# Kernel tuning notes

Measured on AMD Instinct MI355X. Metric: run time of the kernel, lower is better.

## Reference

```python
import jax, jax.numpy as jnp
import numpy as np

B, T, E, H, D = 1, 2048, 1024, 16, 64  # H*D == E required by module


def setup_inputs() -> dict:
    key = jax.random.key(0)
    ks = jax.random.split(key, 9)
    s_in = (2.0 / E) ** 0.5
    return {
        "x": jax.random.normal(ks[0], (B, T, E), jnp.float32),
        "wq": jax.random.normal(ks[1], (H * D, E), jnp.float32) * E ** -0.5,
        "wk": jax.random.normal(ks[2], (H * D, E), jnp.float32) * E ** -0.5,
        "wv": jax.random.normal(ks[3], (H * D, E), jnp.float32) * E ** -0.5,
        "wr": jax.random.normal(ks[4], (H, E, T), jnp.float32) * s_in,
        "wvr": jax.random.normal(ks[5], (H * D, E), jnp.float32) * E ** -0.5,
        "wj": jax.random.normal(ks[6], (E, E), jnp.float32) * E ** -0.5,
        "gate": jnp.zeros((H, 3), jnp.float32),
        "wo": jax.random.normal(ks[7], (E, H * D), jnp.float32) * E ** -0.5,
    }


def reference(x, wq, wk, wv, wr, wvr, wj, gate, wo):
    Bx, Tx, Ex = x.shape
    Hh = wr.shape[0]
    Dd = wq.shape[0] // Hh
    scale = 1.0 / Dd ** 0.5
    neg = -jnp.inf
    mask = jnp.triu(jnp.ones((Tx, Tx), bool), 1)  # True above diagonal

    def heads(w):  # (B,T,H*D) -> (B,H,T,D)
        return (x @ w.T).reshape(Bx, Tx, Hh, Dd).transpose(0, 2, 1, 3)

    # --- branch 1: standard causal QKV attention ---
    q, k, v = heads(wq), heads(wk), heads(wv)
    qkv_attn = jnp.einsum('bhqd,bhkd->bhqk', q, k) * scale
    qkv_attn = jnp.where(mask, neg, qkv_attn)
    qkv_out = jnp.einsum('bhqk,bhkd->bhqd', jax.nn.softmax(qkv_attn, axis=-1), v)

    # --- branch 2: RRPRAM learned per-position scores ---
    rv = heads(wvr)
    r = jnp.einsum('bte,het->bht', x, wr[:, :, :Tx])  # (B,H,T) key scores
    r_attn = jnp.where(mask, neg, (r * scale)[:, :, None, :])  # (B,H,T,T)
    rrp_out = jnp.einsum('bhqk,bhkd->bhqd', jax.nn.softmax(r_attn, axis=-1), rv)

    # --- branch 3: Janus self-resonance ---
    echo = x @ wj.T            # (B,T,E)
    echo_back = echo @ wj      # F.linear(echo, wj.weight.T)
    scores = (x * echo_back).sum(-1) / Ex ** 0.5  # (B,T)
    j_attn = jnp.where(mask, neg, scores[:, :, None] * scores[:, None, :])  # (B,T,T)
    jA = jax.nn.softmax(j_attn, axis=-1)
    j_val = echo.reshape(Bx, Tx, Hh, Dd).transpose(0, 2, 1, 3)
    jan_out = jnp.einsum('bqk,bhkd->bhqd', jA, j_val)

    # --- gated combine + output proj ---
    g = jax.nn.softmax(gate, axis=-1)  # (H,3)
    out = (g[:, 0][None, :, None, None] * qkv_out
           + g[:, 1][None, :, None, None] * rrp_out
           + g[:, 2][None, :, None, None] * jan_out)
    out = out.transpose(0, 2, 1, 3).reshape(Bx, Tx, Hh * Dd)
    return out @ wo.T
```

## Files before the change

kernel.cpp:

```cpp
#include <hip/hip_runtime.h>
#include <cstddef>
#include <cstdint>

#define TT 2048
#define EE 1024
#define HH 16

typedef unsigned short ushort;
typedef unsigned int uint;
typedef __attribute__((ext_vector_type(8))) short short8;
typedef __attribute__((ext_vector_type(8))) _Float16 half8;
typedef __attribute__((ext_vector_type(4))) float f32x4;
typedef __attribute__((ext_vector_type(4))) ushort ushort4v;

__device__ __forceinline__ ushort f2bf(float f) {
  uint u = __builtin_bit_cast(uint, f);
  u = (u + 0x7FFFu + ((u >> 16) & 1u)) >> 16;
  return (ushort)u;
}
__device__ __forceinline__ float bf2f(ushort h) {
  return __builtin_bit_cast(float, (uint)h << 16);
}

__device__ __forceinline__ void async16(ushort* lds, const ushort* g) {
  __builtin_amdgcn_global_load_lds(
      reinterpret_cast<const __attribute__((address_space(1))) void*>(
          reinterpret_cast<uintptr_t>(g)),
      reinterpret_cast<__attribute__((address_space(3))) void*>(
          static_cast<unsigned int>(reinterpret_cast<uintptr_t>(lds))),
      16, 0, 0);
}

__global__ __launch_bounds__(256) void cvt_x_k(
    const float* __restrict__ in, ushort* __restrict__ obf,
    ushort* __restrict__ oh, float* __restrict__ snorm, int n) {
  if (blockIdx.x == 0) {
    for (int i = threadIdx.x; i < TT; i += 256) snorm[i] = 0.f;
  }
  int i = (blockIdx.x * 256 + threadIdx.x) * 4;
  if (i >= n) return;
  float4 v = *(const float4*)(in + i);
  ushort4v b, h;
  b.x = f2bf(v.x); b.y = f2bf(v.y); b.z = f2bf(v.z); b.w = f2bf(v.w);
  h.x = __builtin_bit_cast(ushort, (_Float16)v.x);
  h.y = __builtin_bit_cast(ushort, (_Float16)v.y);
  h.z = __builtin_bit_cast(ushort, (_Float16)v.z);
  h.w = __builtin_bit_cast(ushort, (_Float16)v.w);
  *(ushort4v*)(obf + i) = b;
  *(ushort4v*)(oh + i) = h;
}

__global__ __launch_bounds__(256) void cvt_w_k(
    const float* __restrict__ s0, const float* __restrict__ s1,
    const float* __restrict__ s2, const float* __restrict__ s3,
    const float* __restrict__ s4, const float* __restrict__ s5,
    ushort* __restrict__ d0, ushort* __restrict__ d1,
    ushort* __restrict__ d2, ushort* __restrict__ d3,
    ushort* __restrict__ d4, ushort* __restrict__ d5, int n) {
  const int which = blockIdx.y;
  const float* src; ushort* dst;
  switch (which) {
    case 0: src = s0; dst = d0; break;
    case 1: src = s1; dst = d1; break;
    case 2: src = s2; dst = d2; break;
    case 3: src = s3; dst = d3; break;
    case 4: src = s4; dst = d4; break;
    default: src = s5; dst = d5; break;
  }
  int i = (blockIdx.x * 256 + threadIdx.x) * 4;
  if (i >= n) return;
  float4 v = *(const float4*)(src + i);
  ushort4v o;
  if (which == 5) {
    o.x = __builtin_bit_cast(ushort, (_Float16)v.x);
    o.y = __builtin_bit_cast(ushort, (_Float16)v.y);
    o.z = __builtin_bit_cast(ushort, (_Float16)v.z);
    o.w = __builtin_bit_cast(ushort, (_Float16)v.w);
  } else {
    o.x = f2bf(v.x); o.y = f2bf(v.y); o.z = f2bf(v.z); o.w = f2bf(v.w);
  }
  *(ushort4v*)(dst + i) = o;
}

__global__ __launch_bounds__(256) void transpose_k(
    const float* __restrict__ in, float* __restrict__ outT, int M, int N)
{
  __shared__ float tile[32][33];
  const int bn = blockIdx.x * 32;
  const int bm = blockIdx.y * 32;
  const int tx = threadIdx.x & 31, ty = threadIdx.x >> 5;
#pragma unroll
  for (int i = 0; i < 32; i += 8)
    tile[ty + i][tx] = in[(size_t)(bm + ty + i) * N + bn + tx];
  __syncthreads();
#pragma unroll
  for (int i = 0; i < 32; i += 8)
    outT[(size_t)(bn + ty + i) * M + bm + tx] = tile[tx][ty + i];
}

__global__ __launch_bounds__(256) void proj5(
    const ushort* __restrict__ Abf, const ushort* __restrict__ Ah,
    const ushort* __restrict__ B0, const ushort* __restrict__ B1,
    const ushort* __restrict__ B2, const ushort* __restrict__ B3,
    const ushort* __restrict__ B4,
    ushort* __restrict__ C0, ushort* __restrict__ C1,
    ushort* __restrict__ C2, ushort* __restrict__ C3,
    ushort* __restrict__ C4, float* __restrict__ snorm,
    int M, int N, int K)
{
  const ushort* A; const ushort* B; ushort* C; int om;
  switch (blockIdx.z) {
    case 0: A = Abf; B = B0; C = C0; om = 1; break;
    case 1: A = Abf; B = B1; C = C1; om = 1; break;
    case 2: A = Abf; B = B2; C = C2; om = 2; break;
    case 3: A = Abf; B = B3; C = C3; om = 1; break;
    default: A = Ah; B = B4; C = C4; om = 3; break;
  }
  const bool f16 = (blockIdx.z == 4);
  __shared__ __align__(16) ushort As[2][128 * 64];
  __shared__ __align__(16) ushort Bs[2][128 * 64];
  const int tid = threadIdx.x;
  const int m0 = blockIdx.y * 128, n0 = blockIdx.x * 128;
  const int w = tid >> 6, lane = tid & 63;
  const int wr = w >> 1, wc = w & 1;
  const int lr = lane & 15, lk = lane >> 4;
  const int srow = lane >> 3;
  const int scol = ((lane & 7) ^ srow) * 8;
  const ushort* AgL = A + (size_t)(m0 + w * 32 + srow) * K + scol;
  const ushort* BgL = B + (size_t)(n0 + w * 32 + srow) * K + scol;
  const int sbase = (w * 32) * 64;
  const int s0 = (lk ^ (lr & 7)) * 8;
  f32x4 acc[4][4] = {};
  const int NT = K >> 6;
#pragma unroll
  for (int c = 0; c < 4; ++c) {
    async16(&As[0][sbase + c * 8 * 64], AgL + (size_t)c * 8 * K);
    async16(&Bs[0][sbase + c * 8 * 64], BgL + (size_t)c * 8 * K);
  }
  __syncthreads();
  for (int kt = 0; kt < NT; ++kt) {
    const int cur = kt & 1;
    if (kt + 1 < NT) {
      const int kn = (kt + 1) << 6;
#pragma unroll
      for (int c = 0; c < 4; ++c) {
        async16(&As[cur ^ 1][sbase + c * 8 * 64], AgL + (size_t)c * 8 * K + kn);
        async16(&Bs[cur ^ 1][sbase + c * 8 * 64], BgL + (size_t)c * 8 * K + kn);
      }
    }
    short8 a0[4], a1[4], b0[4], b1[4];
#pragma unroll
    for (int i = 0; i < 4; ++i) {
      const ushort* p = &As[cur][(wr * 64 + i * 16 + lr) * 64];
      a0[i] = *(const short8*)(p + s0);
      a1[i] = *(const short8*)(p + (s0 ^ 32));
    }
#pragma unroll
    for (int j = 0; j < 4; ++j) {
      const ushort* p = &Bs[cur][(wc * 64 + j * 16 + lr) * 64];
      b0[j] = *(const short8*)(p + s0);
      b1[j] = *(const short8*)(p + (s0 ^ 32));
    }
    if (f16) {
#pragma unroll
      for (int i = 0; i < 4; ++i)
#pragma unroll
        for (int j = 0; j < 4; ++j) {
          acc[i][j] = __builtin_amdgcn_mfma_f32_16x16x32_f16(
              __builtin_bit_cast(half8, a0[i]), __builtin_bit_cast(half8, b0[j]),
              acc[i][j], 0, 0, 0);
          acc[i][j] = __builtin_amdgcn_mfma_f32_16x16x32_f16(
              __builtin_bit_cast(half8, a1[i]), __builtin_bit_cast(half8, b1[j]),
              acc[i][j], 0, 0, 0);
        }
    } else {
#pragma unroll
      for (int i = 0; i < 4; ++i)
#pragma unroll
        for (int j = 0; j < 4; ++j) {
          acc[i][j] = __builtin_amdgcn_mfma_f32_16x16x32_bf16(
              a0[i], b0[j], acc[i][j], 0, 0, 0);
          acc[i][j] = __builtin_amdgcn_mfma_f32_16x16x32_bf16(
              a1[i], b1[j], acc[i][j], 0, 0, 0);
        }
    }
    __syncthreads();
  }
#pragma unroll
  for (int i = 0; i < 4; ++i)
#pragma unroll
    for (int r = 0; r < 4; ++r) {
      int row = m0 + wr * 64 + i * 16 + lk * 4 + r;
#pragma unroll
      for (int j = 0; j < 4; ++j) {
        int col = n0 + wc * 64 + j * 16 + lr;
        ushort v = f2bf(acc[i][j][r]);
        if (om == 1)
          C[((size_t)(col >> 6) * M + row) * 64 + (col & 63)] = v;
        else if (om == 2)
          C[(size_t)(col >> 6) * 64 * M + (size_t)(col & 63) * M + row] = v;
        else
          C[(size_t)col * M + row] = v;
      }
    }
  if (om == 3) {
#pragma unroll
    for (int i = 0; i < 4; ++i)
#pragma unroll
      for (int r = 0; r < 4; ++r) {
        float p = 0.f;
#pragma unroll
        for (int j = 0; j < 4; ++j) p += acc[i][j][r] * acc[i][j][r];
        p += __shfl_xor(p, 1); p += __shfl_xor(p, 2);
        p += __shfl_xor(p, 4); p += __shfl_xor(p, 8);
        if (lr == 0)
          atomicAdd(&snorm[m0 + wr * 64 + i * 16 + lk * 4 + r], p);
      }
  }
}

template<bool CZ>
__global__ __launch_bounds__(256) void gemm_mfma(
    const ushort* __restrict__ A, const ushort* __restrict__ B,
    float* __restrict__ Cp, int M, int N, int K)
{
  __shared__ __align__(16) ushort As[2][128 * 64];
  __shared__ __align__(16) ushort Bs[2][128 * 64];
  const int tid = threadIdx.x;
  const int m0 = blockIdx.y * 128, n0 = blockIdx.x * 128;
  const int w = tid >> 6, lane = tid & 63;
  const int wr = w >> 1, wc = w & 1;
  const int lr = lane & 15, lk = lane >> 4;
  const int srow = lane >> 3;
  const int scol = ((lane & 7) ^ srow) * 8;
  const ushort* AgL = A + (size_t)(m0 + w * 32 + srow) * K + scol;
  const ushort* BgL = B + (size_t)(n0 + w * 32 + srow) * K + scol;
  const int sbase = (w * 32) * 64;
  const int s0 = (lk ^ (lr & 7)) * 8;
  f32x4 acc[4][4] = {};
  const int Keff = CZ ? (K < m0 + 128 ? K : m0 + 128) : K;
  const int NT = Keff >> 6;
#pragma unroll
  for (int c = 0; c < 4; ++c) {
    async16(&As[0][sbase + c * 8 * 64], AgL + (size_t)c * 8 * K);
    async16(&Bs[0][sbase + c * 8 * 64], BgL + (size_t)c * 8 * K);
  }
  __syncthreads();
  for (int kt = 0; kt < NT; ++kt) {
    const int cur = kt & 1;
    if (kt + 1 < NT) {
      const int kn = (kt + 1) << 6;
#pragma unroll
      for (int c = 0; c < 4; ++c) {
        async16(&As[cur ^ 1][sbase + c * 8 * 64], AgL + (size_t)c * 8 * K + kn);
        async16(&Bs[cur ^ 1][sbase + c * 8 * 64], BgL + (size_t)c * 8 * K + kn);
      }
    }
    short8 a0[4], a1[4], b0[4], b1[4];
#pragma unroll
    for (int i = 0; i < 4; ++i) {
      const ushort* p = &As[cur][(wr * 64 + i * 16 + lr) * 64];
      a0[i] = *(const short8*)(p + s0);
      a1[i] = *(const short8*)(p + (s0 ^ 32));
    }
#pragma unroll
    for (int j = 0; j < 4; ++j) {
      const ushort* p = &Bs[cur][(wc * 64 + j * 16 + lr) * 64];
      b0[j] = *(const short8*)(p + s0);
      b1[j] = *(const short8*)(p + (s0 ^ 32));
    }
#pragma unroll
    for (int i = 0; i < 4; ++i)
#pragma unroll
      for (int j = 0; j < 4; ++j) {
        acc[i][j] = __builtin_amdgcn_mfma_f32_16x16x32_bf16(
            a0[i], b0[j], acc[i][j], 0, 0, 0);
        acc[i][j] = __builtin_amdgcn_mfma_f32_16x16x32_bf16(
            a1[i], b1[j], acc[i][j], 0, 0, 0);
      }
    __syncthreads();
  }
#pragma unroll
  for (int i = 0; i < 4; ++i)
#pragma unroll
    for (int r = 0; r < 4; ++r) {
      int row = m0 + wr * 64 + i * 16 + lk * 4 + r;
#pragma unroll
      for (int j = 0; j < 4; ++j) {
        int col = n0 + wc * 64 + j * 16 + lr;
        Cp[(size_t)row * N + col] = acc[i][j][r];
      }
    }
}

__global__ __launch_bounds__(256) void flash_mfma(
    const ushort* __restrict__ Qg, const ushort* __restrict__ Kg,
    const ushort* __restrict__ Vg, float* __restrict__ pbuf, int T, int nqt)
{
  const int h = blockIdx.x;
  const int qt = nqt - 1 - blockIdx.y;
  const int sp = blockIdx.z;
  const int q0 = qt * 64;
  const int nk = qt + 1;
  const int span = (nk + 1) >> 1;
  const int kb = sp * span;
  const int ke = (nk < kb + span) ? nk : (kb + span);
  const int tid = threadIdx.x, w = tid >> 6, lane = tid & 63;
  const int lr = lane & 15, lk = lane >> 4;
  const ushort* Q = Qg + (size_t)h * T * 64;
  const ushort* K = Kg + (size_t)h * T * 64;
  const ushort* V = Vg + (size_t)h * 64 * T;
  __shared__ __align__(16) ushort Ps[4][16 * 72];
  const float CEXP = 0.18033688f;

  f32x4 o[4] = {};
  float ls[4] = {0.f, 0.f, 0.f, 0.f};

  if (kb < ke) {
    short8 qa0 = *(const short8*)(Q + (size_t)(q0 + w * 16 + lr) * 64 + lk * 8);
    short8 qa1 = *(const short8*)(Q + (size_t)(q0 + w * 16 + lr) * 64 + 32 + lk * 8);
    short8 kb0[4], kb1[4];
#pragma unroll
    for (int c = 0; c < 4; ++c) {
      const ushort* kp = K + (size_t)(kb * 64 + c * 16 + lr) * 64 + lk * 8;
      kb0[c] = *(const short8*)kp;
      kb1[c] = *(const short8*)(kp + 32);
    }
    for (int kt = kb; kt < ke; ++kt) {
      const int k0 = kt * 64;
      short8 vb0[4], vb1[4];
#pragma unroll
      for (int c = 0; c < 4; ++c) {
        const ushort* vp = V + (size_t)(c * 16 + lr) * T + k0 + lk * 8;
        vb0[c] = *(const short8*)vp;
        vb1[c] = *(const short8*)(vp + 32);
      }
      f32x4 s[4];
#pragma unroll
      for (int c = 0; c < 4; ++c) {
        f32x4 z = {};
        z = __builtin_amdgcn_mfma_f32_16x16x32_bf16(qa0, kb0[c], z, 0, 0, 0);
        z = __builtin_amdgcn_mfma_f32_16x16x32_bf16(qa1, kb1[c], z, 0, 0, 0);
        s[c] = z;
      }
      if (kt + 1 < ke) {
#pragma unroll
        for (int c = 0; c < 4; ++c) {
          const ushort* kp = K + (size_t)(k0 + 64 + c * 16 + lr) * 64 + lk * 8;
          kb0[c] = *(const short8*)kp;
          kb1[c] = *(const short8*)(kp + 32);
        }
      }
      const bool diag = (kt == qt);
      const int rowbase = q0 + w * 16 + lk * 4;
#pragma unroll
      for (int c = 0; c < 4; ++c) {
        const int col = k0 + c * 16 + lr;
#pragma unroll
        for (int r = 0; r < 4; ++r) {
          float p = exp2f(s[c][r] * CEXP);
          if (diag && col > rowbase + r) p = 0.f;
          ls[r] += p;
          Ps[w][(lk * 4 + r) * 72 + c * 16 + lr] = f2bf(p);
        }
      }
      short8 pa0 = *(const short8*)(&Ps[w][lr * 72 + lk * 8]);
      short8 pa1 = *(const short8*)(&Ps[w][lr * 72 + 32 + lk * 8]);
#pragma unroll
      for (int c = 0; c < 4; ++c) {
        o[c] = __builtin_amdgcn_mfma_f32_16x16x32_bf16(pa0, vb0[c], o[c], 0, 0, 0);
        o[c] = __builtin_amdgcn_mfma_f32_16x16x32_bf16(pa1, vb1[c], o[c], 0, 0, 0);
      }
    }
#pragma unroll
    for (int r = 0; r < 4; ++r) {
      ls[r] += __shfl_xor(ls[r], 1);
      ls[r] += __shfl_xor(ls[r], 2);
      ls[r] += __shfl_xor(ls[r], 4);
      ls[r] += __shfl_xor(ls[r], 8);
    }
  }
  float* pb = pbuf + ((size_t)(h * nqt + qt) * 2 + sp) * 4160;
#pragma unroll
  for (int c = 0; c < 4; ++c)
#pragma unroll
    for (int r = 0; r < 4; ++r) {
      int row = w * 16 + lk * 4 + r;
      pb[(size_t)row * 64 + c * 16 + lr] = o[c][r];
    }
  if (lr == 0) {
#pragma unroll
    for (int r = 0; r < 4; ++r)
      pb[4096 + w * 16 + lk * 4 + r] = ls[r];
  }
}

__global__ __launch_bounds__(256) void flash_merge(
    const float* __restrict__ pbuf, ushort* __restrict__ O, int T, int nqt)
{
  const int b = blockIdx.x;
  const int h = b / nqt, qt = b - h * nqt;
  const float* p0 = pbuf + (size_t)b * 2 * 4160;
  const float* p1 = p0 + 4160;
  ushort* Oh = O + ((size_t)h * T + qt * 64) * 64;
  __shared__ float lsum[64];
  if (threadIdx.x < 64)
    lsum[threadIdx.x] = p0[4096 + threadIdx.x] + p1[4096 + threadIdx.x];
  __syncthreads();
  for (int i = threadIdx.x; i < 4096; i += 256) {
    int r = i >> 6;
    Oh[i] = f2bf((p0[i] + p1[i]) / lsum[r]);
  }
}

__global__ __launch_bounds__(256) void rscore3(
    const float* __restrict__ xT, const float* __restrict__ wr,
    float* __restrict__ rpart, int T, int E)
{
  const int h = blockIdx.y;
  const int e0 = blockIdx.z * 64;
  const int t0 = (blockIdx.x * 256 + threadIdx.x) * 4;
  const float* wrh = wr + (size_t)h * E * T;
  float4 acc = {0.f, 0.f, 0.f, 0.f};
#pragma unroll 4
  for (int e = e0; e < e0 + 64; ++e) {
    float4 xv = *(const float4*)(xT + (size_t)e * T + t0);
    float4 wv = *(const float4*)(wrh + (size_t)e * T + t0);
    acc.x += xv.x * wv.x;
    acc.y += xv.y * wv.y;
    acc.z += xv.z * wv.z;
    acc.w += xv.w * wv.w;
  }
  *(float4*)(rpart + ((size_t)blockIdx.z * HH + h) * T + t0) = acc;
}

__global__ __launch_bounds__(256) void rsoftmax2(
    const float* __restrict__ rpart, float* __restrict__ w, int T)
{
  const int h = blockIdx.x;
  __shared__ float rs[TT];
  __shared__ float red[4];
  for (int t = threadIdx.x; t < T; t += 256) {
    float a = 0.f;
#pragma unroll
    for (int s = 0; s < 16; ++s) a += rpart[((size_t)s * HH + h) * T + t];
    rs[t] = a;
  }
  __syncthreads();
  float mx = -1e30f;
  for (int t = threadIdx.x; t < T; t += 256) mx = fmaxf(mx, rs[t]);
#pragma unroll
  for (int o = 32; o; o >>= 1) mx = fmaxf(mx, __shfl_xor(mx, o));
  if ((threadIdx.x & 63) == 0) red[threadIdx.x >> 6] = mx;
  __syncthreads();
  mx = fmaxf(fmaxf(red[0], red[1]), fmaxf(red[2], red[3]));
  float* wh = w + (size_t)h * T;
  for (int t = threadIdx.x; t < T; t += 256)
    wh[t] = __expf((rs[t] - mx) * 0.125f);
}

__global__ __launch_bounds__(64) void rrp_part(
    const float* __restrict__ wgt, const ushort* __restrict__ rv,
    float* __restrict__ segsum, int T)
{
  const int h = blockIdx.x, seg = blockIdx.y, d = threadIdx.x;
  const int segLen = T >> 5;
  const float* wh = wgt + (size_t)h * T;
  const ushort* rvh = rv + (size_t)h * T * 64;
  const int kbeg = seg * segLen, kend = kbeg + segLen;
  float num = 0.f, den = 0.f;
  for (int k = kbeg; k < kend; ++k) {
    float wk = wh[k];
    num += wk * bf2f(rvh[(size_t)k * 64 + d]);
    den += wk;
  }
  float* o = segsum + ((size_t)h * 32 + seg) * 65;
  o[d] = num;
  if (d == 0) o[64] = den;
}

__global__ __launch_bounds__(64) void rrp_scan2(
    const float* __restrict__ wgt, const ushort* __restrict__ rv,
    const float* __restrict__ segsum, ushort* __restrict__ out, int T)
{
  const int h = blockIdx.x, seg = blockIdx.y, d = threadIdx.x;
  const int segLen = T >> 5;
  const float* wh = wgt + (size_t)h * T;
  const ushort* rvh = rv + (size_t)h * T * 64;
  ushort* oh = out + (size_t)h * T * 64;
  float num = 0.f, den = 0.f;
  for (int s = 0; s < seg; ++s) {
    const float* p = segsum + ((size_t)h * 32 + s) * 65;
    num += p[d];
    den += p[64];
  }
  const int kbeg = seg * segLen, kend = kbeg + segLen;
  for (int k = kbeg; k < kend; ++k) {
    float wk = wh[k];
    num += wk * bf2f(rvh[(size_t)k * 64 + d]);
    den += wk;
    oh[(size_t)k * 64 + d] = f2bf(num / den);
  }
}

__global__ __launch_bounds__(256) void janus_w(
    const float* __restrict__ snorm, ushort* __restrict__ Wb,
    float* __restrict__ den, int T)
{
  const int q = blockIdx.x;
  const float sq = snorm[q] * 0.03125f;
  float mx = -1e30f;
  for (int k = threadIdx.x; k <= q; k += 256)
    mx = fmaxf(mx, sq * (snorm[k] * 0.03125f));
#pragma unroll
  for (int o = 32; o; o >>= 1) mx = fmaxf(mx, __shfl_xor(mx, o));
  __shared__ float red[4];
  if ((threadIdx.x & 63) == 0) red[threadIdx.x >> 6] = mx;
  __syncthreads();
  mx = fmaxf(fmaxf(red[0], red[1]), fmaxf(red[2], red[3]));
  float sum = 0.f;
  ushort* Wq = Wb + (size_t)q * T;
  for (int k = threadIdx.x; k < T; k += 256) {
    float wv = (k <= q) ? __expf(sq * (snorm[k] * 0.03125f) - mx) : 0.f;
    ushort wb = f2bf(wv);
    Wq[k] = wb;
    sum += bf2f(wb);
  }
#pragma unroll
  for (int o = 32; o; o >>= 1) sum += __shfl_xor(sum, o);
  __syncthreads();
  if ((threadIdx.x & 63) == 0) red[threadIdx.x >> 6] = sum;
  __syncthreads();
  if (threadIdx.x == 0) den[q] = red[0] + red[1] + red[2] + red[3];
}

__global__ __launch_bounds__(256) void combine_kernel(
    const ushort* __restrict__ a1, const ushort* __restrict__ a2,
    const float* __restrict__ jraw, const float* __restrict__ denj,
    const float* __restrict__ gate, ushort* __restrict__ comb, int T)
{
  const int idx = blockIdx.x * 256 + threadIdx.x;
  const int t = idx >> 10;
  const int c = idx & 1023;
  const int h = c >> 6;
  const int d = c & 63;
  float g0 = gate[h * 3 + 0], g1 = gate[h * 3 + 1], g2 = gate[h * 3 + 2];
  float mg = fmaxf(g0, fmaxf(g1, g2));
  float e0 = __expf(g0 - mg), e1 = __expf(g1 - mg), e2 = __expf(g2 - mg);
  float inv = 1.f / (e0 + e1 + e2);
  const size_t hd = ((size_t)h * T + t) * 64 + d;
  float v = (e0 * bf2f(a1[hd]) + e1 * bf2f(a2[hd]) + e2 * jraw[idx] / denj[t]) * inv;
  comb[idx] = f2bf(v);
}

extern "C" void kernel_launch(void* const* d_in, const int* in_sizes, int n_in,
                              void* d_out, int out_size, void* d_ws, size_t ws_size,
                              hipStream_t stream)
{
  (void)in_sizes; (void)n_in; (void)out_size; (void)ws_size;
  const float* x    = (const float*)d_in[0];
  const float* wq   = (const float*)d_in[1];
  const float* wk   = (const float*)d_in[2];
  const float* wv   = (const float*)d_in[3];
  const float* wr   = (const float*)d_in[4];
  const float* wvr  = (const float*)d_in[5];
  const float* wj   = (const float*)d_in[6];
  const float* gate = (const float*)d_in[7];
  const float* wo   = (const float*)d_in[8];
  float* out = (float*)d_out;

  const int T = TT, E = EE, H = HH;
  const int nqt = T / 64;
  const size_t TE = (size_t)T * E;
  const size_t EE2 = (size_t)E * E;
  const size_t TT2 = (size_t)T * T;

  ushort* u = (ushort*)d_ws;
  ushort* xbf   = u;
  ushort* xh    = xbf + TE;
  ushort* wqb   = xh + TE;
  ushort* wkb   = wqb + EE2;
  ushort* wvb   = wkb + EE2;
  ushort* wvrb  = wvb + EE2;
  ushort* wob   = wvrb + EE2;
  ushort* wjh   = wob + EE2;
  ushort* qhb   = wjh + EE2;
  ushort* khb   = qhb + TE;
  ushort* vtb   = khb + TE;
  ushort* rvhb  = vtb + TE;
  ushort* echoT = rvhb + TE;
  ushort* a1b   = echoT + TE;
  ushort* a2b   = a1b + TE;
  ushort* Wbf   = a2b + TE;
  ushort* combb = Wbf + TT2;
  float* jraw   = (float*)(combb + TE);
  float* wwb    = jraw + TE;
  float* snorm  = wwb + (size_t)H * T;
  float* denj   = snorm + T;
  float* rpart  = denj + T;
  float* segsum = rpart + (size_t)16 * H * T;
  float* xT     = segsum + (size_t)H * 32 * 65;
  float* pbuf   = xT + TE;

  dim3 blk(256);
  cvt_x_k<<<(int)(TE / 1024), blk, 0, stream>>>(x, xbf, xh, snorm, (int)TE);
  cvt_w_k<<<dim3((int)(EE2 / 1024), 6), blk, 0, stream>>>(
      wq, wk, wv, wvr, wo, wj, wqb, wkb, wvb, wvrb, wob, wjh, (int)EE2);
  transpose_k<<<dim3(E / 32, T / 32), blk, 0, stream>>>(x, xT, T, E);

  proj5<<<dim3(E / 128, T / 128, 5), blk, 0, stream>>>(
      xbf, xh, wqb, wkb, wvb, wvrb, wjh,
      qhb, khb, vtb, rvhb, echoT, snorm, T, E, E);

  rscore3<<<dim3(T / 1024, H, 16), blk, 0, stream>>>(xT, wr, rpart, T, E);
  rsoftmax2<<<H, blk, 0, stream>>>(rpart, wwb, T);

  flash_mfma<<<dim3(H, nqt, 2), blk, 0, stream>>>(qhb, khb, vtb, pbuf, T, nqt);
  flash_merge<<<H * nqt, blk, 0, stream>>>(pbuf, a1b, T, nqt);

  rrp_part<<<dim3(H, 32), dim3(64), 0, stream>>>(wwb, rvhb, segsum, T);
  rrp_scan2<<<dim3(H, 32), dim3(64), 0, stream>>>(wwb, rvhb, segsum, a2b, T);

  janus_w<<<T, blk, 0, stream>>>(snorm, Wbf, denj, T);
  gemm_mfma<true><<<dim3(E / 128, T / 128), blk, 0, stream>>>(
      Wbf, echoT, jraw, T, E, T);

  combine_kernel<<<(int)(TE / 256), blk, 0, stream>>>(a1b, a2b, jraw, denj,
                                                      gate, combb, T);
  gemm_mfma<false><<<dim3(E / 128, T / 128), blk, 0, stream>>>(
      combb, wob, (float*)out, T, E, E);
}
```

Baseline: 458.3 us.

## Split causal flash attention four ways with XCD-aware block mapping and MFMA priority

The causal flash-attention kernel now splits each query tile's key range into four partitions instead of two. It uses a flattened 1D grid whose block index maps two heads onto each of the eight XCDs, so blocks of the same head share an L2. The QK and PV MFMA sections are wrapped in s_setprio to favour matrix work over the surrounding loads and exp. The merge kernel now sums four partial outputs and row sums, which doubles the partial-buffer traffic and footprint; if the workspace was sized for two splits, this could overrun it.

After: 459.6 us. About the same (+0.3%).

```diff
diff --git a/kernel.cpp b/kernel.cpp
--- a/kernel.cpp
+++ b/kernel.cpp
@@ -5,6 +5,7 @@
 #define TT 2048
 #define EE 1024
 #define HH 16
+#define NSP 4
 
 typedef unsigned short ushort;
 typedef unsigned int uint;
@@ -297,12 +298,16 @@
     const ushort* __restrict__ Qg, const ushort* __restrict__ Kg,
     const ushort* __restrict__ Vg, float* __restrict__ pbuf, int T, int nqt)
 {
-  const int h = blockIdx.x;
-  const int qt = nqt - 1 - blockIdx.y;
-  const int sp = blockIdx.z;
+  const int bid = blockIdx.x;
+  const int xcd = bid & 7;
+  const int jj = bid >> 3;
+  const int h = xcd * 2 + (jj & 1);
+  const int rest = jj >> 1;
+  const int sp = rest & 3;
+  const int qt = (nqt - 1) - (rest >> 2);
   const int q0 = qt * 64;
   const int nk = qt + 1;
-  const int span = (nk + 1) >> 1;
+  const int span = (nk + NSP - 1) >> 2;
   const int kb = sp * span;
   const int ke = (nk < kb + span) ? nk : (kb + span);
   const int tid = threadIdx.x, w = tid >> 6, lane = tid & 63;
@@ -336,6 +341,7 @@
         vb1[c] = *(const short8*)(vp + 32);
       }
       f32x4 s[4];
+      __builtin_amdgcn_s_setprio(1);
 #pragma unroll
       for (int c = 0; c < 4; ++c) {
         f32x4 z = {};
@@ -343,6 +349,7 @@
         z = __builtin_amdgcn_mfma_f32_16x16x32_bf16(qa1, kb1[c], z, 0, 0, 0);
         s[c] = z;
       }
+      __builtin_amdgcn_s_setprio(0);
       if (kt + 1 < ke) {
 #pragma unroll
         for (int c = 0; c < 4; ++c) {
@@ -366,11 +373,13 @@
       }
       short8 pa0 = *(const short8*)(&Ps[w][lr * 72 + lk * 8]);
       short8 pa1 = *(const short8*)(&Ps[w][lr * 72 + 32 + lk * 8]);
+      __builtin_amdgcn_s_setprio(1);
 #pragma unroll
       for (int c = 0; c < 4; ++c) {
         o[c] = __builtin_amdgcn_mfma_f32_16x16x32_bf16(pa0, vb0[c], o[c], 0, 0, 0);
         o[c] = __builtin_amdgcn_mfma_f32_16x16x32_bf16(pa1, vb1[c], o[c], 0, 0, 0);
       }
+      __builtin_amdgcn_s_setprio(0);
     }
 #pragma unroll
     for (int r = 0; r < 4; ++r) {
@@ -380,7 +389,7 @@
       ls[r] += __shfl_xor(ls[r], 8);
     }
   }
-  float* pb = pbuf + ((size_t)(h * nqt + qt) * 2 + sp) * 4160;
+  float* pb = pbuf + ((size_t)(h * nqt + qt) * NSP + sp) * 4160;
 #pragma unroll
   for (int c = 0; c < 4; ++c)
 #pragma unroll
@@ -400,16 +409,19 @@
 {
   const int b = blockIdx.x;
   const int h = b / nqt, qt = b - h * nqt;
-  const float* p0 = pbuf + (size_t)b * 2 * 4160;
+  const float* p0 = pbuf + (size_t)b * NSP * 4160;
   const float* p1 = p0 + 4160;
+  const float* p2 = p1 + 4160;
+  const float* p3 = p2 + 4160;
   ushort* Oh = O + ((size_t)h * T + qt * 64) * 64;
   __shared__ float lsum[64];
   if (threadIdx.x < 64)
-    lsum[threadIdx.x] = p0[4096 + threadIdx.x] + p1[4096 + threadIdx.x];
+    lsum[threadIdx.x] = p0[4096 + threadIdx.x] + p1[4096 + threadIdx.x] +
+                        p2[4096 + threadIdx.x] + p3[4096 + threadIdx.x];
   __syncthreads();
   for (int i = threadIdx.x; i < 4096; i += 256) {
     int r = i >> 6;
-    Oh[i] = f2bf((p0[i] + p1[i]) / lsum[r]);
+    Oh[i] = f2bf((p0[i] + p1[i] + p2[i] + p3[i]) / lsum[r]);
   }
 }
 
@@ -615,7 +627,7 @@
   rscore3<<<dim3(T / 1024, H, 16), blk, 0, stream>>>(xT, wr, rpart, T, E);
   rsoftmax2<<<H, blk, 0, stream>>>(rpart, wwb, T);
 
-  flash_mfma<<<dim3(H, nqt, 2), blk, 0, stream>>>(qhb, khb, vtb, pbuf, T, nqt);
+  flash_mfma<<<dim3(H * nqt * NSP), blk, 0, stream>>>(qhb, khb, vtb, pbuf, T, nqt);
   flash_merge<<<H * nqt, blk, 0, stream>>>(pbuf, a1b, T, nqt);
 
   rrp_part<<<dim3(H, 32), dim3(64), 0, stream>>>(wwb, rvhb, segsum, T);
```
